# Performance work log

Hardware: AMD Instinct MI355X
Metric: run time of the kernel (lower is better)

## Reference

```python
import jax, jax.numpy as jnp
import numpy as np

N = 100000   # nodes
D = 128      # embedding_dim
E = 1600000  # edges
L = 3        # num_layers


def setup_inputs() -> dict:
    key = jax.random.key(0)
    ks = jax.random.split(key, 10)
    s = 1.0 / np.sqrt(D)
    def w(k, shape):
        return jax.random.uniform(k, shape, jnp.float32, -s, s)
    return {
        "x": jax.random.normal(ks[0], (N, D), jnp.float32),
        "edge_index": jax.random.randint(ks[1], (2, E), 0, N, jnp.int32),
        "Wp": w(ks[2], (L - 1, D, D)),   # project Linear weight (per layer)
        "bp": w(ks[3], (L - 1, D)),      # project Linear bias
        "Wl": w(ks[4], (L - 1, D, D)),   # lin_l (aggregated neighbors)
        "bl": w(ks[5], (L - 1, D)),
        "Wr": w(ks[6], (L - 1, D, D)),   # lin_r (root, no bias)
        "Wl_out": w(ks[7], (D, D)),
        "bl_out": w(ks[8], (D,)),
        "Wr_out": w(ks[9], (D, D)),
    }


def _sage(x, src, dst, inv_deg, Wl, bl, Wr, Wp=None, bp=None, normalize=False):
    # PyG SAGEConv: project applies to messages only; root term uses original x.
    h = jax.nn.relu(x @ Wp.T + bp) if Wp is not None else x
    agg = jax.ops.segment_sum(h[src], dst, num_segments=N) * inv_deg  # mean aggr
    out = agg @ Wl.T + bl + x @ Wr.T
    if normalize:
        out = out / jnp.maximum(
            jnp.linalg.norm(out, axis=-1, keepdims=True), 1e-12)
    return out


def reference(x, edge_index, Wp, bp, Wl, bl, Wr, Wl_out, bl_out, Wr_out):
    src, dst = edge_index[0], edge_index[1]
    deg = jax.ops.segment_sum(jnp.ones((src.shape[0],), x.dtype), dst,
                              num_segments=N)
    inv_deg = (1.0 / jnp.maximum(deg, 1.0))[:, None]  # isolated nodes -> 0 agg
    for i in range(L - 1):
        x = jax.nn.relu(
            _sage(x, src, dst, inv_deg, Wl[i], bl[i], Wr[i], Wp[i], bp[i],
                  normalize=True))
    return _sage(x, src, dst, inv_deg, Wl_out, bl_out, Wr_out)
```

## Files before the change

### kernel.cpp

```cpp
#include <hip/hip_runtime.h>
#include <math.h>

#define D 128
#define BCAP 5120

typedef short s8v __attribute__((ext_vector_type(8)));
typedef float f32x4 __attribute__((ext_vector_type(4)));
typedef unsigned short u16x8 __attribute__((ext_vector_type(8)));

__device__ __forceinline__ unsigned short f2bf(float f) {
  union { float f; unsigned u; } c; c.f = f;
  unsigned u = c.u;
  unsigned r = (u + 0x7fffu + ((u >> 16) & 1u)) >> 16;
  return (unsigned short)r;
}

__device__ __forceinline__ void gload_lds16(const void* g, void* l) {
  __builtin_amdgcn_global_load_lds((const __attribute__((address_space(1))) void*)g,
                                   (__attribute__((address_space(3))) void*)l, 16, 0, 0);
}

__device__ __forceinline__ int swz_chunk(int r, int c) { return (r << 4) + (c ^ (r & 7)); }

__global__ __launch_bounds__(1024, 2) void k_partA_cvt(const int* __restrict__ src,
                                                       const int* __restrict__ dst,
                                                       int* __restrict__ cursor,
                                                       unsigned* __restrict__ pairs, int E_,
                                                       const float* __restrict__ Wp,
                                                       const float* __restrict__ Wl,
                                                       const float* __restrict__ Wr,
                                                       const float* __restrict__ Wlo,
                                                       const float* __restrict__ Wro,
                                                       unsigned short* __restrict__ Wb,
                                                       int nA) {
  __shared__ int hist[512];
  __shared__ int gbase[512];
  __shared__ int lim[512];
  int t = threadIdx.x;

  if ((int)blockIdx.x < nA) {
    int base = blockIdx.x * 16384;
    if (t < 512) hist[t] = 0;
    __syncthreads();
    unsigned p_[16];
    int k_[16];
#pragma unroll
    for (int i = 0; i < 16; i++) {
      int e = base + i * 1024 + t;
      if (e < E_) {
        int s = src[e], d = dst[e];
        p_[i] = ((unsigned)s << 8) | (unsigned)(d & 255);
        k_[i] = d >> 8;
        atomicAdd(&hist[k_[i]], 1);
      } else {
        k_[i] = -1;
      }
    }
    __syncthreads();
    if (t < 512) {
      int c = hist[t];
      int start = c ? atomicAdd(&cursor[t], c) : 0;
      gbase[t] = t * BCAP + start;
      lim[t] = BCAP - start;
      hist[t] = 0;
    }
    __syncthreads();
#pragma unroll
    for (int i = 0; i < 16; i++) {
      if (k_[i] >= 0) {
        int r = atomicAdd(&hist[k_[i]], 1);
        if (r < lim[k_[i]]) pairs[gbase[k_[i]] + r] = p_[i];
      }
    }
  } else {
    int i = ((int)blockIdx.x - nA) * 1024 + t;
    const float* s;
    int off;
    if (i < 8192)       { s = Wp;  off = 0; }
    else if (i < 16384) { s = Wl;  off = 8192; }
    else if (i < 24576) { s = Wr;  off = 16384; }
    else if (i < 28672) { s = Wlo; off = 24576; }
    else                { s = Wro; off = 28672; }
    float4 a = ((const float4*)s)[i - off];
    ushort4 o;
    o.x = f2bf(a.x); o.y = f2bf(a.y); o.z = f2bf(a.z); o.w = f2bf(a.w);
    ((ushort4*)Wb)[i] = o;
  }
}

__global__ __launch_bounds__(1024, 2) void k_partB_proj(const unsigned* __restrict__ pairs,
                                                        const int* __restrict__ bcnt,
                                                        int* __restrict__ csrCursor,
                                                        int* __restrict__ row_start,
                                                        int* __restrict__ deg,
                                                        int* __restrict__ csr,
                                                        const float* __restrict__ Av,
                                                        const unsigned short* __restrict__ W,
                                                        const float* __restrict__ bias,
                                                        unsigned short* __restrict__ out,
                                                        unsigned short* __restrict__ xb_out,
                                                        int n, int nB) {
  __shared__ __align__(16) unsigned short Wlds[128 * 128];
  __shared__ int cnt[256];
  __shared__ int scn[256];
  __shared__ int baseSh;
  int t = threadIdx.x;

  if ((int)blockIdx.x < nB) {
    int k = blockIdx.x;
    int node0 = k << 8;
    int len = bcnt[k];
    if (len > BCAP) len = BCAP;
    const unsigned* pb = pairs + (size_t)k * BCAP;
    if (t == 0) baseSh = atomicAdd(csrCursor, len);
    if (t < 256) cnt[t] = 0;
    __syncthreads();
    for (int p = t; p < len; p += 1024) atomicAdd(&cnt[pb[p] & 255], 1);
    __syncthreads();
    int c = 0;
    if (t < 256) { c = cnt[t]; scn[t] = c; }
    __syncthreads();
    for (int off = 1; off < 256; off <<= 1) {
      int xv = 0;
      if (t < 256 && t >= off) xv = scn[t - off];
      __syncthreads();
      if (t < 256) scn[t] += xv;
      __syncthreads();
    }
    if (t < 256) {
      int ex = scn[t] - c;
      int node = node0 + t;
      if (node < n) { row_start[node] = baseSh + ex; deg[node] = c; }
      cnt[t] = baseSh + ex;
    }
    __syncthreads();
    for (int p = t; p < len; p += 1024) {
      unsigned pr = pb[p];
      int slot = atomicAdd(&cnt[pr & 255], 1);
      csr[slot] = (int)(pr >> 8);
    }
  } else {
    int bid = blockIdx.x - nB;
    int wv = t >> 6, l = t & 63, lg = l >> 4, ln = l & 15;
    int rb = bid * 256 + wv * 16;
    int arow = rb + ln;
    if (arow >= n) arow = n - 1;

    s8v a[4];
    const float* Af = Av + (size_t)arow * D + lg * 8;
#pragma unroll
    for (int ks = 0; ks < 4; ++ks) {
      float4 f0 = *(const float4*)(Af + ks * 32);
      float4 f1 = *(const float4*)(Af + ks * 32 + 4);
      s8v av;
      av[0] = (short)f2bf(f0.x); av[1] = (short)f2bf(f0.y);
      av[2] = (short)f2bf(f0.z); av[3] = (short)f2bf(f0.w);
      av[4] = (short)f2bf(f1.x); av[5] = (short)f2bf(f1.y);
      av[6] = (short)f2bf(f1.z); av[7] = (short)f2bf(f1.w);
      a[ks] = av;
      *(s8v*)(xb_out + (size_t)arow * D + lg * 8 + ks * 32) = av;
    }

#pragma unroll
    for (int i = 0; i < 2; ++i) {
      int idx = t + i * 1024;
      int r = idx >> 4, k = idx & 15;
      int c = k ^ (r & 7);
      gload_lds16(W + r * 128 + c * 8, &Wlds[idx * 8]);
    }
    __syncthreads();

    f32x4 acc[8];
#pragma unroll
    for (int f = 0; f < 8; ++f) acc[f] = (f32x4){0.f, 0.f, 0.f, 0.f};
#pragma unroll
    for (int ks = 0; ks < 4; ++ks) {
#pragma unroll
      for (int f = 0; f < 8; ++f) {
        s8v b = *(const s8v*)&Wlds[swz_chunk(f * 16 + ln, ks * 4 + lg) * 8];
        acc[f] = __builtin_amdgcn_mfma_f32_16x16x32_bf16(a[ks], b, acc[f], 0, 0, 0);
      }
    }

#pragma unroll
    for (int r = 0; r < 4; ++r) {
      int gr = rb + 4 * lg + r;
      if (gr < n) {
#pragma unroll
        for (int f = 0; f < 8; ++f) {
          int c = f * 16 + ln;
          float v = acc[f][r] + bias[c];
          v = fmaxf(v, 0.f);
          out[(size_t)gr * D + c] = f2bf(v);
        }
      }
    }
  }
}

__global__ __launch_bounds__(256) void k_aggregate(const unsigned short* __restrict__ h,
                                                   unsigned short* __restrict__ agg,
                                                   const int* __restrict__ row_start,
                                                   const int* __restrict__ deg,
                                                   const int* __restrict__ csr, int n) {
  int node = (blockIdx.x * 256 + threadIdx.x) >> 4;
  int li = threadIdx.x & 15;
  if (node >= n) return;
  int rs0 = row_start[node];
  int dc = deg[node];
  const int* ce = csr + rs0;
  const char* base = (const char*)h + li * 16;

  float accL[4], accH[4];
#pragma unroll
  for (int q = 0; q < 4; q++) { accL[q] = 0.f; accH[q] = 0.f; }

#define ACCR(v)                                                        \
  {                                                                    \
    unsigned dw[4] = {(v).x, (v).y, (v).z, (v).w};                     \
    _Pragma("unroll") for (int q = 0; q < 4; q++) {                    \
      accL[q] += __uint_as_float(dw[q] << 16);                         \
      accH[q] += __uint_as_float(dw[q] & 0xffff0000u);                 \
    }                                                                  \
  }

  int e = 0;
  bool more = (3 < dc);
  int s0 = 0, s1 = 0, s2 = 0, s3 = 0;
  if (more) { s0 = ce[0]; s1 = ce[1]; s2 = ce[2]; s3 = ce[3]; }
  while (more) {
    uint4 v0 = *(const uint4*)(base + (size_t)s0 * 256);
    uint4 v1 = *(const uint4*)(base + (size_t)s1 * 256);
    uint4 v2 = *(const uint4*)(base + (size_t)s2 * 256);
    uint4 v3 = *(const uint4*)(base + (size_t)s3 * 256);
    e += 4;
    more = (e + 3 < dc);
    if (more) { s0 = ce[e]; s1 = ce[e + 1]; s2 = ce[e + 2]; s3 = ce[e + 3]; }
    ACCR(v0); ACCR(v1); ACCR(v2); ACCR(v3);
  }
  if (e < dc)     { uint4 v = *(const uint4*)(base + (size_t)ce[e] * 256);     ACCR(v); }
  if (e + 1 < dc) { uint4 v = *(const uint4*)(base + (size_t)ce[e + 1] * 256); ACCR(v); }
  if (e + 2 < dc) { uint4 v = *(const uint4*)(base + (size_t)ce[e + 2] * 256); ACCR(v); }
#undef ACCR

  float iv = 1.0f / (float)(dc > 0 ? dc : 1);
  u16x8 o;
#pragma unroll
  for (int q = 0; q < 4; q++) {
    o[2 * q] = f2bf(accL[q] * iv);
    o[2 * q + 1] = f2bf(accH[q] * iv);
  }
  *(u16x8*)(agg + (size_t)node * D + li * 8) = o;
}

template <int MODE>
__global__ __launch_bounds__(512, 4) void k_gemm_dual(const unsigned short* __restrict__ A1,
                                                      const unsigned short* __restrict__ W1,
                                                      const float* __restrict__ bias,
                                                      const unsigned short* __restrict__ A2,
                                                      const unsigned short* __restrict__ W2,
                                                      void* __restrict__ outv, int n) {
  __shared__ __align__(16) unsigned short Wlds[2 * 128 * 128];
  int t = threadIdx.x;
  int wv = t >> 6, l = t & 63, lg = l >> 4, ln = l & 15;
  int rb = blockIdx.x * 128 + wv * 16;
  int arow = rb + ln;
  if (arow >= n) arow = n - 1;
  const s8v* A1p = (const s8v*)(A1 + (size_t)arow * D + lg * 8);
  const s8v* A2p = (const s8v*)(A2 + (size_t)arow * D + lg * 8);
  s8v a1[4], a2[4];
#pragma unroll
  for (int ks = 0; ks < 4; ++ks) { a1[ks] = A1p[ks * 4]; a2[ks] = A2p[ks * 4]; }

#pragma unroll
  for (int i = 0; i < 8; ++i) {
    int idx = t + i * 512;
    int mat = idx >> 11;
    int rem = idx & 2047;
    int r = rem >> 4, k = rem & 15;
    int c = k ^ (r & 7);
    const unsigned short* src = (mat ? W2 : W1) + r * 128 + c * 8;
    gload_lds16(src, &Wlds[idx * 8]);
  }
  __syncthreads();

  f32x4 acc[8];
#pragma unroll
  for (int f = 0; f < 8; ++f) acc[f] = (f32x4){0.f, 0.f, 0.f, 0.f};

#pragma unroll
  for (int ks = 0; ks < 4; ++ks) {
#pragma unroll
    for (int f = 0; f < 8; ++f) {
      int ch = swz_chunk(f * 16 + ln, ks * 4 + lg) * 8;
      s8v b1 = *(const s8v*)&Wlds[ch];
      s8v b2 = *(const s8v*)&Wlds[16384 + ch];
      acc[f] = __builtin_amdgcn_mfma_f32_16x16x32_bf16(a1[ks], b1, acc[f], 0, 0, 0);
      acc[f] = __builtin_amdgcn_mfma_f32_16x16x32_bf16(a2[ks], b2, acc[f], 0, 0, 0);
    }
  }

#pragma unroll
  for (int r = 0; r < 4; ++r) {
    int gr = rb + 4 * lg + r;
    float v[8];
#pragma unroll
    for (int f = 0; f < 8; ++f) v[f] = acc[f][r] + bias[f * 16 + ln];
    if (MODE == 0) {
      float ss = 0.f;
#pragma unroll
      for (int f = 0; f < 8; ++f) ss += v[f] * v[f];
      ss += __shfl_xor(ss, 1);
      ss += __shfl_xor(ss, 2);
      ss += __shfl_xor(ss, 4);
      ss += __shfl_xor(ss, 8);
      float sc = 1.0f / fmaxf(sqrtf(ss), 1e-12f);
      if (gr < n) {
        unsigned short* out = (unsigned short*)outv;
#pragma unroll
        for (int f = 0; f < 8; ++f) {
          float o = fmaxf(v[f] * sc, 0.f);
          out[(size_t)gr * D + f * 16 + ln] = f2bf(o);
        }
      }
    } else {
      if (gr < n) {
        float* out = (float*)outv;
#pragma unroll
        for (int f = 0; f < 8; ++f) out[(size_t)gr * D + f * 16 + ln] = v[f];
      }
    }
  }
}

__global__ __launch_bounds__(512, 4) void k_dual_proj(const unsigned short* __restrict__ A1,
                                                      const unsigned short* __restrict__ W1,
                                                      const float* __restrict__ bias,
                                                      const unsigned short* __restrict__ A2,
                                                      const unsigned short* __restrict__ W2,
                                                      unsigned short* __restrict__ x1out,
                                                      const unsigned short* __restrict__ Wp,
                                                      const float* __restrict__ biasP,
                                                      unsigned short* __restrict__ hout,
                                                      int n) {
  __shared__ __align__(16) unsigned short Wlds[2 * 128 * 128];
  int t = threadIdx.x;
  int wv = t >> 6, l = t & 63, lg = l >> 4, ln = l & 15;
  int rb = blockIdx.x * 128 + wv * 16;
  int arow = rb + ln;
  if (arow >= n) arow = n - 1;
  const s8v* A1p = (const s8v*)(A1 + (size_t)arow * D + lg * 8);
  const s8v* A2p = (const s8v*)(A2 + (size_t)arow * D + lg * 8);
  s8v a1[4], a2[4];
#pragma unroll
  for (int ks = 0; ks < 4; ++ks) { a1[ks] = A1p[ks * 4]; a2[ks] = A2p[ks * 4]; }

#pragma unroll
  for (int i = 0; i < 8; ++i) {
    int idx = t + i * 512;
    int mat = idx >> 11;
    int rem = idx & 2047;
    int r = rem >> 4, k = rem & 15;
    int c = k ^ (r & 7);
    const unsigned short* src = (mat ? W2 : W1) + r * 128 + c * 8;
    gload_lds16(src, &Wlds[idx * 8]);
  }
  __syncthreads();

  f32x4 acc[8];
#pragma unroll
  for (int f = 0; f < 8; ++f) acc[f] = (f32x4){0.f, 0.f, 0.f, 0.f};
#pragma unroll
  for (int ks = 0; ks < 4; ++ks) {
#pragma unroll
    for (int f = 0; f < 8; ++f) {
      int ch = swz_chunk(f * 16 + ln, ks * 4 + lg) * 8;
      s8v b1 = *(const s8v*)&Wlds[ch];
      s8v b2 = *(const s8v*)&Wlds[16384 + ch];
      acc[f] = __builtin_amdgcn_mfma_f32_16x16x32_bf16(a1[ks], b1, acc[f], 0, 0, 0);
      acc[f] = __builtin_amdgcn_mfma_f32_16x16x32_bf16(a2[ks], b2, acc[f], 0, 0, 0);
    }
  }
  __syncthreads();

#pragma unroll
  for (int i = 0; i < 4; ++i) {
    int idx = t + i * 512;
    int r = idx >> 4, k = idx & 15;
    int c = k ^ (r & 7);
    gload_lds16(Wp + r * 128 + c * 8, &Wlds[idx * 8]);
  }

#pragma unroll
  for (int r = 0; r < 4; ++r) {
    int gr = rb + 4 * lg + r;
    float v[8];
#pragma unroll
    for (int f = 0; f < 8; ++f) v[f] = acc[f][r] + bias[f * 16 + ln];
    float ss = 0.f;
#pragma unroll
    for (int f = 0; f < 8; ++f) ss += v[f] * v[f];
    ss += __shfl_xor(ss, 1);
    ss += __shfl_xor(ss, 2);
    ss += __shfl_xor(ss, 4);
    ss += __shfl_xor(ss, 8);
    float sc = 1.0f / fmaxf(sqrtf(ss), 1e-12f);
    if (gr < n) {
#pragma unroll
      for (int f = 0; f < 8; ++f) {
        float o = fmaxf(v[f] * sc, 0.f);
        x1out[(size_t)gr * D + f * 16 + ln] = f2bf(o);
      }
    }
  }

  asm volatile("s_waitcnt vmcnt(0)" ::: "memory");
  __builtin_amdgcn_sched_barrier(0);
  __syncthreads();

  const s8v* Xp = (const s8v*)(x1out + (size_t)arow * D + lg * 8);
  s8v ap[4];
#pragma unroll
  for (int ks = 0; ks < 4; ++ks) ap[ks] = Xp[ks * 4];

  f32x4 acc2[8];
#pragma unroll
  for (int f = 0; f < 8; ++f) acc2[f] = (f32x4){0.f, 0.f, 0.f, 0.f};
#pragma unroll
  for (int ks = 0; ks < 4; ++ks) {
#pragma unroll
    for (int f = 0; f < 8; ++f) {
      s8v b = *(const s8v*)&Wlds[swz_chunk(f * 16 + ln, ks * 4 + lg) * 8];
      acc2[f] = __builtin_amdgcn_mfma_f32_16x16x32_bf16(ap[ks], b, acc2[f], 0, 0, 0);
    }
  }

#pragma unroll
  for (int r = 0; r < 4; ++r) {
    int gr = rb + 4 * lg + r;
    if (gr < n) {
#pragma unroll
      for (int f = 0; f < 8; ++f) {
        int c = f * 16 + ln;
        float v = acc2[f][r] + biasP[c];
        v = fmaxf(v, 0.f);
        hout[(size_t)gr * D + c] = f2bf(v);
      }
    }
  }
}

extern "C" void kernel_launch(void* const* d_in, const int* in_sizes, int n_in,
                              void* d_out, int out_size, void* d_ws, size_t ws_size,
                              hipStream_t stream) {
  const float* x   = (const float*)d_in[0];
  const int*   ei  = (const int*)d_in[1];
  const float* Wp  = (const float*)d_in[2];
  const float* bp  = (const float*)d_in[3];
  const float* Wl  = (const float*)d_in[4];
  const float* bl  = (const float*)d_in[5];
  const float* Wr  = (const float*)d_in[6];
  const float* Wlo = (const float*)d_in[7];
  const float* blo = (const float*)d_in[8];
  const float* Wro = (const float*)d_in[9];

  const int N = in_sizes[0] / D;
  const int E = in_sizes[1] / 2;
  const int* srcIdx = ei;
  const int* dstIdx = ei + E;

  const size_t ND = (size_t)N * D;

  unsigned short* xb   = (unsigned short*)d_ws;
  unsigned short* h    = xb + ND;
  unsigned short* aggB = h + ND;
  unsigned short* x2   = aggB + ND;
  unsigned short* Wb   = x2 + ND;
  int* row_start  = (int*)(Wb + 8 * 16384);
  int* degA       = row_start + N;
  int* cursor     = degA + N;
  int* csrCursor  = cursor + 512;
  int* csr        = csrCursor + 1;

  unsigned* pairs = (unsigned*)aggB;

  unsigned short* Wpb0 = Wb;
  unsigned short* Wpb1 = Wb + 16384;
  unsigned short* Wlb0 = Wb + 2 * 16384;
  unsigned short* Wlb1 = Wb + 3 * 16384;
  unsigned short* Wrb0 = Wb + 4 * 16384;
  unsigned short* Wrb1 = Wb + 5 * 16384;
  unsigned short* Wlob = Wb + 6 * 16384;
  unsigned short* Wrob = Wb + 7 * 16384;

  unsigned short* x1 = (unsigned short*)d_out;

  int gG  = (N + 127) / 128;
  int gP  = (N + 255) / 256;
  int gAg = (N * 16 + 255) / 256;
  int KB  = (N + 255) / 256;
  int gA  = (E + 16383) / 16384;

  hipMemsetAsync(cursor, 0, 513 * sizeof(int), stream);

  k_partA_cvt<<<gA + 32, 1024, 0, stream>>>(srcIdx, dstIdx, cursor, pairs, E,
                                            Wp, Wl, Wr, Wlo, Wro, Wb, gA);

  k_partB_proj<<<KB + gP, 1024, 0, stream>>>(pairs, cursor, csrCursor,
                                             row_start, degA, csr,
                                             x, Wpb0, bp, h, xb, N, KB);

  k_aggregate<<<gAg, 256, 0, stream>>>(h, aggB, row_start, degA, csr, N);
  k_dual_proj<<<gG, 512, 0, stream>>>(aggB, Wlb0, bl, xb, Wrb0, x1,
                                      Wpb1, bp + D, h, N);

  k_aggregate<<<gAg, 256, 0, stream>>>(h, aggB, row_start, degA, csr, N);
  k_gemm_dual<0><<<gG, 512, 0, stream>>>(aggB, Wlb1, bl + D, x1, Wrb1, (void*)x2, N);

  k_aggregate<<<gAg, 256, 0, stream>>>(x2, aggB, row_start, degA, csr, N);
  k_gemm_dual<1><<<gG, 512, 0, stream>>>(aggB, Wlob, blo, x2, Wrob, d_out, N);
}
```

Baseline: 307.6 us.

## Move first projection into bucketing kernel and stage x1 tile in LDS

The layer-0 projection GEMM now runs in the same launch as edge bucketing and weight conversion. It converts Wp to bf16 in-kernel, so it no longer depends on the separate conversion pass. CSR construction is split into its own kernel, and the block sizes change to 512 threads. In the dual projection kernel, the normalized x1 tile is written into LDS and reread from there for the next GEMM, instead of going through global memory behind a vmcnt wait. This overlaps independent work and removes a global round trip, at the cost of redundant per-block weight conversion and more LDS use.

```diff
diff --git a/kernel.cpp b/kernel.cpp
--- a/kernel.cpp
+++ b/kernel.cpp
@@ -22,7 +22,7 @@
 
 __device__ __forceinline__ int swz_chunk(int r, int c) { return (r << 4) + (c ^ (r & 7)); }
 
-__global__ __launch_bounds__(1024, 2) void k_partA_cvt(const int* __restrict__ src,
+__global__ __launch_bounds__(512, 4) void k_build_proj(const int* __restrict__ src,
                                                        const int* __restrict__ dst,
                                                        int* __restrict__ cursor,
                                                        unsigned* __restrict__ pairs, int E_,
@@ -32,21 +32,27 @@
                                                        const float* __restrict__ Wlo,
                                                        const float* __restrict__ Wro,
                                                        unsigned short* __restrict__ Wb,
-                                                       int nA) {
+                                                       const float* __restrict__ Av,
+                                                       const float* __restrict__ bias,
+                                                       unsigned short* __restrict__ hout,
+                                                       unsigned short* __restrict__ xb_out,
+                                                       int n, int nA, int nC) {
+  __shared__ __align__(16) unsigned short Wlds[128 * 128];
   __shared__ int hist[512];
   __shared__ int gbase[512];
   __shared__ int lim[512];
   int t = threadIdx.x;
-
-  if ((int)blockIdx.x < nA) {
-    int base = blockIdx.x * 16384;
-    if (t < 512) hist[t] = 0;
+  int bid = blockIdx.x;
+
+  if (bid < nA) {
+    int base = bid * 8192;
+    hist[t] = 0;
     __syncthreads();
     unsigned p_[16];
     int k_[16];
 #pragma unroll
     for (int i = 0; i < 16; i++) {
-      int e = base + i * 1024 + t;
+      int e = base + i * 512 + t;
       if (e < E_) {
         int s = src[e], d = dst[e];
         p_[i] = ((unsigned)s << 8) | (unsigned)(d & 255);
@@ -57,7 +63,7 @@
       }
     }
     __syncthreads();
-    if (t < 512) {
+    {
       int c = hist[t];
       int start = c ? atomicAdd(&cursor[t], c) : 0;
       gbase[t] = t * BCAP + start;
@@ -72,8 +78,8 @@
         if (r < lim[k_[i]]) pairs[gbase[k_[i]] + r] = p_[i];
       }
     }
-  } else {
-    int i = ((int)blockIdx.x - nA) * 1024 + t;
+  } else if (bid < nA + nC) {
+    int i = 4096 + (bid - nA) * 512 + t;
     const float* s;
     int off;
     if (i < 8192)       { s = Wp;  off = 0; }
@@ -85,66 +91,26 @@
     ushort4 o;
     o.x = f2bf(a.x); o.y = f2bf(a.y); o.z = f2bf(a.z); o.w = f2bf(a.w);
     ((ushort4*)Wb)[i] = o;
-  }
-}
-
-__global__ __launch_bounds__(1024, 2) void k_partB_proj(const unsigned* __restrict__ pairs,
-                                                        const int* __restrict__ bcnt,
-                                                        int* __restrict__ csrCursor,
-                                                        int* __restrict__ row_start,
-                                                        int* __restrict__ deg,
-                                                        int* __restrict__ csr,
-                                                        const float* __restrict__ Av,
-                                                        const unsigned short* __restrict__ W,
-                                                        const float* __restrict__ bias,
-                                                        unsigned short* __restrict__ out,
-                                                        unsigned short* __restrict__ xb_out,
-                                                        int n, int nB) {
-  __shared__ __align__(16) unsigned short Wlds[128 * 128];
-  __shared__ int cnt[256];
-  __shared__ int scn[256];
-  __shared__ int baseSh;
-  int t = threadIdx.x;
-
-  if ((int)blockIdx.x < nB) {
-    int k = blockIdx.x;
-    int node0 = k << 8;
-    int len = bcnt[k];
-    if (len > BCAP) len = BCAP;
-    const unsigned* pb = pairs + (size_t)k * BCAP;
-    if (t == 0) baseSh = atomicAdd(csrCursor, len);
-    if (t < 256) cnt[t] = 0;
-    __syncthreads();
-    for (int p = t; p < len; p += 1024) atomicAdd(&cnt[pb[p] & 255], 1);
-    __syncthreads();
-    int c = 0;
-    if (t < 256) { c = cnt[t]; scn[t] = c; }
-    __syncthreads();
-    for (int off = 1; off < 256; off <<= 1) {
-      int xv = 0;
-      if (t < 256 && t >= off) xv = scn[t - off];
-      __syncthreads();
-      if (t < 256) scn[t] += xv;
-      __syncthreads();
-    }
-    if (t < 256) {
-      int ex = scn[t] - c;
-      int node = node0 + t;
-      if (node < n) { row_start[node] = baseSh + ex; deg[node] = c; }
-      cnt[t] = baseSh + ex;
-    }
-    __syncthreads();
-    for (int p = t; p < len; p += 1024) {
-      unsigned pr = pb[p];
-      int slot = atomicAdd(&cnt[pr & 255], 1);
-      csr[slot] = (int)(pr >> 8);
-    }
   } else {
-    int bid = blockIdx.x - nB;
+    int pbid = bid - nA - nC;
     int wv = t >> 6, l = t & 63, lg = l >> 4, ln = l & 15;
-    int rb = bid * 256 + wv * 16;
+    int rb = pbid * 128 + wv * 16;
     int arow = rb + ln;
     if (arow >= n) arow = n - 1;
+
+#pragma unroll
+    for (int i = 0; i < 4; ++i) {
+      int idx = t + i * 512;
+      int r = idx >> 4, k = idx & 15;
+      int c = k ^ (r & 7);
+      const float* wsrc = Wp + r * 128 + c * 8;
+      float4 f0 = *(const float4*)wsrc;
+      float4 f1 = *(const float4*)(wsrc + 4);
+      u16x8 wb;
+      wb[0] = f2bf(f0.x); wb[1] = f2bf(f0.y); wb[2] = f2bf(f0.z); wb[3] = f2bf(f0.w);
+      wb[4] = f2bf(f1.x); wb[5] = f2bf(f1.y); wb[6] = f2bf(f1.z); wb[7] = f2bf(f1.w);
+      *(u16x8*)&Wlds[idx * 8] = wb;
+    }
 
     s8v a[4];
     const float* Af = Av + (size_t)arow * D + lg * 8;
@@ -160,14 +126,6 @@
       a[ks] = av;
       *(s8v*)(xb_out + (size_t)arow * D + lg * 8 + ks * 32) = av;
     }
-
-#pragma unroll
-    for (int i = 0; i < 2; ++i) {
-      int idx = t + i * 1024;
-      int r = idx >> 4, k = idx & 15;
-      int c = k ^ (r & 7);
-      gload_lds16(W + r * 128 + c * 8, &Wlds[idx * 8]);
-    }
     __syncthreads();
 
     f32x4 acc[8];
@@ -191,10 +149,53 @@
           int c = f * 16 + ln;
           float v = acc[f][r] + bias[c];
           v = fmaxf(v, 0.f);
-          out[(size_t)gr * D + c] = f2bf(v);
+          hout[(size_t)gr * D + c] = f2bf(v);
         }
       }
     }
+  }
+}
+
+__global__ __launch_bounds__(1024) void k_partB(const unsigned* __restrict__ pairs,
+                                                const int* __restrict__ bcnt,
+                                                int* __restrict__ csrCursor,
+                                                int* __restrict__ row_start,
+                                                int* __restrict__ deg,
+                                                int* __restrict__ csr, int n) {
+  __shared__ int cnt[256];
+  __shared__ int scn[256];
+  __shared__ int baseSh;
+  int k = blockIdx.x, t = threadIdx.x;
+  int node0 = k << 8;
+  int len = bcnt[k];
+  if (len > BCAP) len = BCAP;
+  const unsigned* pb = pairs + (size_t)k * BCAP;
+  if (t == 0) baseSh = atomicAdd(csrCursor, len);
+  if (t < 256) cnt[t] = 0;
+  __syncthreads();
+  for (int p = t; p < len; p += 1024) atomicAdd(&cnt[pb[p] & 255], 1);
+  __syncthreads();
+  int c = 0;
+  if (t < 256) { c = cnt[t]; scn[t] = c; }
+  __syncthreads();
+  for (int off = 1; off < 256; off <<= 1) {
+    int xv = 0;
+    if (t < 256 && t >= off) xv = scn[t - off];
+    __syncthreads();
+    if (t < 256) scn[t] += xv;
+    __syncthreads();
+  }
+  if (t < 256) {
+    int ex = scn[t] - c;
+    int node = node0 + t;
+    if (node < n) { row_start[node] = baseSh + ex; deg[node] = c; }
+    cnt[t] = baseSh + ex;
+  }
+  __syncthreads();
+  for (int p = t; p < len; p += 1024) {
+    unsigned pr = pb[p];
+    int slot = atomicAdd(&cnt[pr & 255], 1);
+    csr[slot] = (int)(pr >> 8);
   }
 }
 
@@ -394,6 +395,7 @@
 #pragma unroll
   for (int r = 0; r < 4; ++r) {
     int gr = rb + 4 * lg + r;
+    int lrow = wv * 16 + 4 * lg + r;
     float v[8];
 #pragma unroll
     for (int f = 0; f < 8; ++f) v[f] = acc[f][r] + bias[f * 16 + ln];
@@ -405,23 +407,23 @@
     ss += __shfl_xor(ss, 4);
     ss += __shfl_xor(ss, 8);
     float sc = 1.0f / fmaxf(sqrtf(ss), 1e-12f);
-    if (gr < n) {
-#pragma unroll
-      for (int f = 0; f < 8; ++f) {
-        float o = fmaxf(v[f] * sc, 0.f);
-        x1out[(size_t)gr * D + f * 16 + ln] = f2bf(o);
-      }
-    }
-  }
-
-  asm volatile("s_waitcnt vmcnt(0)" ::: "memory");
-  __builtin_amdgcn_sched_barrier(0);
-  __syncthreads();
-
-  const s8v* Xp = (const s8v*)(x1out + (size_t)arow * D + lg * 8);
+#pragma unroll
+    for (int f = 0; f < 8; ++f) {
+      float o = fmaxf(v[f] * sc, 0.f);
+      unsigned short ob = f2bf(o);
+      int col = f * 16 + ln;
+      Wlds[16384 + swz_chunk(lrow, col >> 3) * 8 + (col & 7)] = ob;
+      if (gr < n) x1out[(size_t)gr * D + col] = ob;
+    }
+  }
+
+  __syncthreads();
+
+  int lrow2 = wv * 16 + ln;
   s8v ap[4];
 #pragma unroll
-  for (int ks = 0; ks < 4; ++ks) ap[ks] = Xp[ks * 4];
+  for (int ks = 0; ks < 4; ++ks)
+    ap[ks] = *(const s8v*)&Wlds[16384 + swz_chunk(lrow2, ks * 4 + lg) * 8];
 
   f32x4 acc2[8];
 #pragma unroll
@@ -484,7 +486,6 @@
 
   unsigned* pairs = (unsigned*)aggB;
 
-  unsigned short* Wpb0 = Wb;
   unsigned short* Wpb1 = Wb + 16384;
   unsigned short* Wlb0 = Wb + 2 * 16384;
   unsigned short* Wlb1 = Wb + 3 * 16384;
@@ -496,19 +497,18 @@
   unsigned short* x1 = (unsigned short*)d_out;
 
   int gG  = (N + 127) / 128;
-  int gP  = (N + 255) / 256;
   int gAg = (N * 16 + 255) / 256;
   int KB  = (N + 255) / 256;
-  int gA  = (E + 16383) / 16384;
+  int gA  = (E + 8191) / 8192;
+  int nC  = 56;
 
   hipMemsetAsync(cursor, 0, 513 * sizeof(int), stream);
 
-  k_partA_cvt<<<gA + 32, 1024, 0, stream>>>(srcIdx, dstIdx, cursor, pairs, E,
-                                            Wp, Wl, Wr, Wlo, Wro, Wb, gA);
-
-  k_partB_proj<<<KB + gP, 1024, 0, stream>>>(pairs, cursor, csrCursor,
-                                             row_start, degA, csr,
-                                             x, Wpb0, bp, h, xb, N, KB);
+  k_build_proj<<<gA + nC + gG, 512, 0, stream>>>(srcIdx, dstIdx, cursor, pairs, E,
+                                                 Wp, Wl, Wr, Wlo, Wro, Wb,
+                                                 x, bp, h, xb, N, gA, nC);
+
+  k_partB<<<KB, 1024, 0, stream>>>(pairs, cursor, csrCursor, row_start, degA, csr, N);
 
   k_aggregate<<<gAg, 256, 0, stream>>>(h, aggB, row_start, degA, csr, N);
   k_dual_proj<<<gG, 512, 0, stream>>>(aggB, Wlb0, bl, xb, Wrb0, x1,
```

After: 300.3 us, median of 2. 1.02x faster.
